# Optimization experiments

Measured on AMD Instinct MI355X. Metric: run time of the kernel, lower is better.

The kernel has to match this reference:

```python
import jax, jax.numpy as jnp
import numpy as np

EPS = 1e-6

def _phi(x):
    # elu(x) + 1 feature map
    return jax.nn.elu(x) + 1.0

def setup_inputs() -> dict:
    key = jax.random.key(0)
    kq, kk, kv = jax.random.split(key, 3)
    N, L, S, H, D, M = 8, 4096, 4096, 8, 64, 64
    queries = jax.random.normal(kq, (N, L, H, D), dtype=jnp.float32)
    keys = jax.random.normal(kk, (N, S, H, D), dtype=jnp.float32)
    values = jax.random.normal(kv, (N, S, H, M), dtype=jnp.float32)
    key_mask = jnp.ones((N, S), dtype=jnp.float32)  # key_lengths.float_matrix
    return {"queries": queries, "keys": keys, "values": values, "key_mask": key_mask}

def reference(queries, keys, values, key_mask):
    Q = _phi(queries)                                   # [N,L,H,D]
    K = _phi(keys) * key_mask[:, :, None, None]         # [N,S,H,D]
    KV = jnp.einsum('nshd,nshm->nhmd', K, values)       # [N,H,M,D]
    Z = 1.0 / (jnp.einsum('nlhd,nhd->nlh', Q, K.sum(axis=1)) + EPS)  # [N,L,H]
    V = jnp.einsum('nlhd,nhmd,nlh->nlhm', Q, KV, Z)     # [N,L,H,M]
    return V
```

## Files before the change

kernel.cpp:

```cpp
#include <hip/hip_runtime.h>


#define SLEN 4096
#define LLEN 4096
#define NHTOT 64
#define HD   512
#define NSPLIT 8
#define EPSF 1e-6f

typedef short s16x8 __attribute__((ext_vector_type(8)));
typedef float f32x4 __attribute__((ext_vector_type(4)));

__device__ __forceinline__ float phi(float x) {
    return x > 0.0f ? x + 1.0f : __expf(x);
}

__device__ __forceinline__ void fma4(float4& a, float s, const float4& b) {
    a.x = fmaf(s, b.x, a.x);
    a.y = fmaf(s, b.y, a.y);
    a.z = fmaf(s, b.z, a.z);
    a.w = fmaf(s, b.w, a.w);
}

__device__ __forceinline__ void bsplit(float x, short& hi, short& lo) {
    const unsigned bx = __float_as_uint(x);
    hi = (short)(bx >> 16);
    const float hf = __uint_as_float(bx & 0xFFFF0000u);
    lo = (short)(__float_as_uint(x - hf) >> 16);
}

__global__ __launch_bounds__(256, 2)
void la_phase1(const float* __restrict__ Kg, const float* __restrict__ Vg,
               const float* __restrict__ maskg,
               float* __restrict__ KVp, float* __restrict__ Ksump) {
    __shared__ float smem[4][4096];
    __shared__ float ksb[16 * 64];

    const int tid  = threadIdx.x;
    const int w    = tid >> 6;
    const int lane = tid & 63;
    const int nh   = blockIdx.y;
    const int n    = nh >> 3;
    const int h    = nh & 7;
    const int sp   = blockIdx.x;

    const int sr4 = lane >> 4;
    const int c4  = (lane & 15) * 4;
    const int d0  = (lane & 7) * 8;
    const int m0  = (lane >> 3) * 8;

    float* kw = smem[w];
    float* vw = smem[w] + 2048;

    const size_t base = (size_t)n * SLEN * HD + (size_t)h * 64;
    const float* mrow = maskg + (size_t)n * SLEN;
    const int wrow0 = sp * 512 + w * 128;

    float4 acc[8][2];
    #pragma unroll
    for (int i = 0; i < 8; ++i) {
        acc[i][0] = make_float4(0.f, 0.f, 0.f, 0.f);
        acc[i][1] = make_float4(0.f, 0.f, 0.f, 0.f);
    }
    float4 ksp = make_float4(0.f, 0.f, 0.f, 0.f);

    float4 pk[8], pv[8];
    float  pm[8];
    #pragma unroll
    for (int u = 0; u < 8; ++u) {
        const int s = wrow0 + sr4 + u * 4;
        const size_t g = base + (size_t)s * HD + c4;
        pk[u] = *(const float4*)(Kg + g);
        pv[u] = *(const float4*)(Vg + g);
        pm[u] = mrow[s];
    }

    #pragma unroll
    for (int t = 0; t < 4; ++t) {
        #pragma unroll
        for (int u = 0; u < 8; ++u) {
            const int row = sr4 + u * 4;
            float4 kf = pk[u];
            const float mm = pm[u];
            kf.x = phi(kf.x) * mm;
            kf.y = phi(kf.y) * mm;
            kf.z = phi(kf.z) * mm;
            kf.w = phi(kf.w) * mm;
            ksp.x += kf.x; ksp.y += kf.y; ksp.z += kf.z; ksp.w += kf.w;
            *(float4*)&kw[row * 64 + c4] = kf;
            *(float4*)&vw[row * 64 + c4] = pv[u];
        }
        if (t < 3) {
            #pragma unroll
            for (int u = 0; u < 8; ++u) {
                const int s = wrow0 + (t + 1) * 32 + sr4 + u * 4;
                const size_t g = base + (size_t)s * HD + c4;
                pk[u] = *(const float4*)(Kg + g);
                pv[u] = *(const float4*)(Vg + g);
                pm[u] = mrow[s];
            }
        }
        #pragma unroll 4
        for (int s = 0; s < 32; ++s) {
            const float4 ka = *(const float4*)&kw[s * 64 + d0];
            const float4 kz = *(const float4*)&kw[s * 64 + d0 + 4];
            const float4 va = *(const float4*)&vw[s * 64 + m0];
            const float4 vz = *(const float4*)&vw[s * 64 + m0 + 4];
            fma4(acc[0][0], ka.x, va); fma4(acc[0][1], ka.x, vz);
            fma4(acc[1][0], ka.y, va); fma4(acc[1][1], ka.y, vz);
            fma4(acc[2][0], ka.z, va); fma4(acc[2][1], ka.z, vz);
            fma4(acc[3][0], ka.w, va); fma4(acc[3][1], ka.w, vz);
            fma4(acc[4][0], kz.x, va); fma4(acc[4][1], kz.x, vz);
            fma4(acc[5][0], kz.y, va); fma4(acc[5][1], kz.y, vz);
            fma4(acc[6][0], kz.z, va); fma4(acc[6][1], kz.z, vz);
            fma4(acc[7][0], kz.w, va); fma4(acc[7][1], kz.w, vz);
        }
    }

    *(float4*)&ksb[(w * 4 + sr4) * 64 + c4] = ksp;

    #pragma unroll
    for (int di = 0; di < 8; ++di) {
        *(float4*)&smem[w][(d0 + di) * 64 + m0]     = acc[di][0];
        *(float4*)&smem[w][(d0 + di) * 64 + m0 + 4] = acc[di][1];
    }
    __syncthreads();

    float* outp = KVp + ((size_t)sp * NHTOT + nh) * 4096;
    #pragma unroll
    for (int j = 0; j < 4; ++j) {
        const int f = (j * 256 + tid) * 4;
        float4 a  = *(const float4*)&smem[0][f];
        const float4 b1 = *(const float4*)&smem[1][f];
        const float4 b2 = *(const float4*)&smem[2][f];
        const float4 b3 = *(const float4*)&smem[3][f];
        a.x += b1.x + b2.x + b3.x;
        a.y += b1.y + b2.y + b3.y;
        a.z += b1.z + b2.z + b3.z;
        a.w += b1.w + b2.w + b3.w;
        *(float4*)&outp[f] = a;
    }
    if (tid < 64) {
        float ssum = 0.f;
        #pragma unroll
        for (int r = 0; r < 16; ++r) ssum += ksb[r * 64 + tid];
        Ksump[((size_t)sp * NHTOT + nh) * 64 + tid] = ssum;
    }
}

__global__ __launch_bounds__(256)
void la_reduce(const float* __restrict__ KVp, const float* __restrict__ Ksump,
               short* __restrict__ KVThi, short* __restrict__ KVTlo,
               float* __restrict__ Ksum) {
    __shared__ float ld[64 * 20];

    const int nh  = blockIdx.y;
    const int mb  = blockIdx.x * 16;
    const int tid = threadIdx.x;

    const int d    = tid >> 2;
    const int moff = (tid & 3) * 4;
    float4 a = make_float4(0.f, 0.f, 0.f, 0.f);
    #pragma unroll
    for (int s = 0; s < NSPLIT; ++s) {
        const float4 v = *(const float4*)&KVp[((size_t)s * NHTOT + nh) * 4096 + d * 64 + mb + moff];
        a.x += v.x; a.y += v.y; a.z += v.z; a.w += v.w;
    }
    *(float4*)&ld[d * 20 + moff] = a;
    __syncthreads();

    const int mloc = tid >> 4;
    const int d0   = (tid & 15) * 4;
    short hi4[4], lo4[4];
    #pragma unroll
    for (int i = 0; i < 4; ++i)
        bsplit(ld[(d0 + i) * 20 + mloc], hi4[i], lo4[i]);
    const size_t o = (size_t)nh * 4096 + (mb + mloc) * 64 + d0;
    *(short4*)&KVThi[o] = *(short4*)hi4;
    *(short4*)&KVTlo[o] = *(short4*)lo4;

    if (blockIdx.x == 0 && tid < 64) {
        float b = 0.f;
        #pragma unroll
        for (int s = 0; s < NSPLIT; ++s)
            b += Ksump[((size_t)s * NHTOT + nh) * 64 + tid];
        Ksum[nh * 64 + tid] = b;
    }
}

__global__ __launch_bounds__(256)
void la_phase2(const float* __restrict__ Qg,
               const short* __restrict__ KVThi, const short* __restrict__ KVTlo,
               const float* __restrict__ Ksum, float* __restrict__ Og) {
    const int tid  = threadIdx.x;
    const int w    = tid >> 6;
    const int lane = tid & 63;
    const int nh   = blockIdx.y;
    const int n    = nh >> 3;
    const int h    = nh & 7;
    const int l0   = blockIdx.x * 128 + w * 32;

    const int r  = lane & 15;
    const int g4 = lane >> 4;

    const short* bhp = KVThi + (size_t)nh * 4096;
    const short* blp = KVTlo + (size_t)nh * 4096;
    const float* ksp = Ksum + nh * 64;

    f32x4 acc[2][4];
    #pragma unroll
    for (int t = 0; t < 2; ++t)
        #pragma unroll
        for (int u = 0; u < 4; ++u)
            acc[t][u] = (f32x4){0.f, 0.f, 0.f, 0.f};
    float den[2] = {0.f, 0.f};

    #pragma unroll
    for (int g = 0; g < 2; ++g) {
        const int db = g * 32 + g4 * 8;

        s16x8 Bh[4], Bl[4];
        #pragma unroll
        for (int u = 0; u < 4; ++u) {
            Bh[u] = *(const s16x8*)&bhp[(u * 16 + r) * 64 + db];
            Bl[u] = *(const s16x8*)&blp[(u * 16 + r) * 64 + db];
        }
        const float4 k0 = *(const float4*)&ksp[db];
        const float4 k1 = *(const float4*)&ksp[db + 4];

        #pragma unroll
        for (int t = 0; t < 2; ++t) {
            const float* qrow = Qg + ((size_t)(n * LLEN + l0 + t * 16 + r) * 8 + h) * 64 + db;
            float4 q0 = *(const float4*)qrow;
            float4 q1 = *(const float4*)(qrow + 4);
            q0.x = phi(q0.x); q0.y = phi(q0.y); q0.z = phi(q0.z); q0.w = phi(q0.w);
            q1.x = phi(q1.x); q1.y = phi(q1.y); q1.z = phi(q1.z); q1.w = phi(q1.w);

            float dn = den[t];
            dn = fmaf(q0.x, k0.x, dn); dn = fmaf(q0.y, k0.y, dn);
            dn = fmaf(q0.z, k0.z, dn); dn = fmaf(q0.w, k0.w, dn);
            dn = fmaf(q1.x, k1.x, dn); dn = fmaf(q1.y, k1.y, dn);
            dn = fmaf(q1.z, k1.z, dn); dn = fmaf(q1.w, k1.w, dn);
            den[t] = dn;

            s16x8 Ah, Al;
            {
                short hh, ll;
                bsplit(q0.x, hh, ll); Ah[0] = hh; Al[0] = ll;
                bsplit(q0.y, hh, ll); Ah[1] = hh; Al[1] = ll;
                bsplit(q0.z, hh, ll); Ah[2] = hh; Al[2] = ll;
                bsplit(q0.w, hh, ll); Ah[3] = hh; Al[3] = ll;
                bsplit(q1.x, hh, ll); Ah[4] = hh; Al[4] = ll;
                bsplit(q1.y, hh, ll); Ah[5] = hh; Al[5] = ll;
                bsplit(q1.z, hh, ll); Ah[6] = hh; Al[6] = ll;
                bsplit(q1.w, hh, ll); Ah[7] = hh; Al[7] = ll;
            }
            #pragma unroll
            for (int u = 0; u < 4; ++u) {
                acc[t][u] = __builtin_amdgcn_mfma_f32_16x16x32_bf16(Ah, Bh[u], acc[t][u], 0, 0, 0);
                acc[t][u] = __builtin_amdgcn_mfma_f32_16x16x32_bf16(Ah, Bl[u], acc[t][u], 0, 0, 0);
                acc[t][u] = __builtin_amdgcn_mfma_f32_16x16x32_bf16(Al, Bh[u], acc[t][u], 0, 0, 0);
            }
        }
    }

    #pragma unroll
    for (int t = 0; t < 2; ++t) {
        den[t] += __shfl_xor(den[t], 16, 64);
        den[t] += __shfl_xor(den[t], 32, 64);
    }

    #pragma unroll
    for (int t = 0; t < 2; ++t) {
        #pragma unroll
        for (int k = 0; k < 4; ++k) {
            const int ro = g4 * 4 + k;
            const float dk = __shfl(den[t], ro, 64);
            const float z  = 1.0f / (dk + EPSF);
            const int l = l0 + t * 16 + ro;
            float* op = &Og[((size_t)(n * LLEN + l) * 8 + h) * 64 + r];
            #pragma unroll
            for (int u = 0; u < 4; ++u)
                op[u * 16] = acc[t][u][k] * z;
        }
    }
}

extern "C" void kernel_launch(void* const* d_in, const int* in_sizes, int n_in,
                              void* d_out, int out_size, void* d_ws, size_t ws_size,
                              hipStream_t stream) {
    const float* Q    = (const float*)d_in[0];
    const float* K    = (const float*)d_in[1];
    const float* V    = (const float*)d_in[2];
    const float* mask = (const float*)d_in[3];
    float* out = (float*)d_out;

    float* KVp   = (float*)d_ws;
    float* Ksump = KVp + (size_t)NSPLIT * NHTOT * 4096;
    float* Ksum  = Ksump + (size_t)NSPLIT * NHTOT * 64;
    short* KVThi = (short*)(Ksum + NHTOT * 64);
    short* KVTlo = KVThi + (size_t)NHTOT * 4096;

    dim3 g1(NSPLIT, NHTOT);
    la_phase1<<<g1, 256, 0, stream>>>(K, V, mask, KVp, Ksump);

    dim3 gr(4, NHTOT);
    la_reduce<<<gr, 256, 0, stream>>>(KVp, Ksump, KVThi, KVTlo, Ksum);

    dim3 g2(LLEN / 128, NHTOT);
    la_phase2<<<g2, 256, 0, stream>>>(Q, KVThi, KVTlo, Ksum, out);
}
```

Measured before the change: 249.7 us.

## Compute phase-1 K^T V with split-bf16 MFMA instead of scalar FMA

The phase-1 kernel now converts phi(K) and V into hi/lo bf16 pairs and stores them transposed in a swizzled shared-memory layout. It then accumulates the KV outer product with three bf16 MFMA 16x16x32 instructions per tile (hi*hi, hi*lo, lo*hi) in place of the fp32 FMA loop. This moves the dominant reduction onto the matrix cores and approximates fp32 accuracy with a 3-term split, at the cost of extra packing work and shared-memory traffic. Accuracy drops slightly because the lo*lo term is left out.

New measurement: 239.3 us. 4.2% less time.

```diff
diff --git a/kernel.cpp b/kernel.cpp
--- a/kernel.cpp
+++ b/kernel.cpp
@@ -15,13 +15,12 @@
     return x > 0.0f ? x + 1.0f : __expf(x);
 }
 
-__device__ __forceinline__ void fma4(float4& a, float s, const float4& b) {
-    a.x = fmaf(s, b.x, a.x);
-    a.y = fmaf(s, b.y, a.y);
-    a.z = fmaf(s, b.z, a.z);
-    a.w = fmaf(s, b.w, a.w);
-}
-
+__device__ __forceinline__ unsigned pack_hi2(float a, float b) {
+    return (__float_as_uint(a) >> 16) | (__float_as_uint(b) & 0xFFFF0000u);
+}
+__device__ __forceinline__ float bres(float x) {
+    return x - __uint_as_float(__float_as_uint(x) & 0xFFFF0000u);
+}
 __device__ __forceinline__ void bsplit(float x, short& hi, short& lo) {
     const unsigned bx = __float_as_uint(x);
     hi = (short)(bx >> 16);
@@ -44,106 +43,138 @@
     const int h    = nh & 7;
     const int sp   = blockIdx.x;
 
-    const int sr4 = lane >> 4;
-    const int c4  = (lane & 15) * 4;
-    const int d0  = (lane & 7) * 8;
-    const int m0  = (lane >> 3) * 8;
-
-    float* kw = smem[w];
-    float* vw = smem[w] + 2048;
+    const int r  = lane & 15;
+    const int a  = lane >> 4;
+    const int c4 = r * 4;
+
+    char* const wbase = (char*)&smem[w][0];
+    char* const kthi = wbase;
+    char* const ktlo = wbase + 4096;
+    char* const vthi = wbase + 8192;
+    char* const vtlo = wbase + 12288;
 
     const size_t base = (size_t)n * SLEN * HD + (size_t)h * 64;
     const float* mrow = maskg + (size_t)n * SLEN;
     const int wrow0 = sp * 512 + w * 128;
 
-    float4 acc[8][2];
-    #pragma unroll
-    for (int i = 0; i < 8; ++i) {
-        acc[i][0] = make_float4(0.f, 0.f, 0.f, 0.f);
-        acc[i][1] = make_float4(0.f, 0.f, 0.f, 0.f);
-    }
+    const int woff0 = ((((a >> 1) ^ (r & 3)) << 4) | ((a & 1) << 3));
+    const int rkey  = (r >> 2) & 3;
+
+    f32x4 acc[4][4];
+    #pragma unroll
+    for (int i = 0; i < 4; ++i)
+        #pragma unroll
+        for (int j = 0; j < 4; ++j)
+            acc[i][j] = (f32x4){0.f, 0.f, 0.f, 0.f};
     float4 ksp = make_float4(0.f, 0.f, 0.f, 0.f);
 
-    float4 pk[8], pv[8];
-    float  pm[8];
-    #pragma unroll
-    for (int u = 0; u < 8; ++u) {
-        const int s = wrow0 + sr4 + u * 4;
-        const size_t g = base + (size_t)s * HD + c4;
-        pk[u] = *(const float4*)(Kg + g);
-        pv[u] = *(const float4*)(Vg + g);
-        pm[u] = mrow[s];
-    }
+    float4 pk[2][4], pv[2][4];
+    float  pm[2][4];
+    #pragma unroll
+    for (int u = 0; u < 2; ++u)
+        #pragma unroll
+        for (int j = 0; j < 4; ++j) {
+            const int s = wrow0 + u * 16 + a * 4 + j;
+            const size_t g = base + (size_t)s * HD + c4;
+            pk[u][j] = *(const float4*)(Kg + g);
+            pv[u][j] = *(const float4*)(Vg + g);
+            pm[u][j] = mrow[s];
+        }
 
     #pragma unroll
     for (int t = 0; t < 4; ++t) {
         #pragma unroll
-        for (int u = 0; u < 8; ++u) {
-            const int row = sr4 + u * 4;
-            float4 kf = pk[u];
-            const float mm = pm[u];
-            kf.x = phi(kf.x) * mm;
-            kf.y = phi(kf.y) * mm;
-            kf.z = phi(kf.z) * mm;
-            kf.w = phi(kf.w) * mm;
-            ksp.x += kf.x; ksp.y += kf.y; ksp.z += kf.z; ksp.w += kf.w;
-            *(float4*)&kw[row * 64 + c4] = kf;
-            *(float4*)&vw[row * 64 + c4] = pv[u];
+        for (int u = 0; u < 2; ++u) {
+            float4 kf[4];
+            #pragma unroll
+            for (int j = 0; j < 4; ++j) {
+                float4 kq = pk[u][j];
+                const float mm = pm[u][j];
+                kq.x = phi(kq.x) * mm; kq.y = phi(kq.y) * mm;
+                kq.z = phi(kq.z) * mm; kq.w = phi(kq.w) * mm;
+                kf[j] = kq;
+                ksp.x += kq.x; ksp.y += kq.y; ksp.z += kq.z; ksp.w += kq.w;
+            }
+            const int wo = woff0 ^ (u << 5);
+            #pragma unroll
+            for (int i = 0; i < 4; ++i) {
+                const int doff = r * 256 + i * 64 + wo;
+                const float k0 = (&kf[0].x)[i], k1 = (&kf[1].x)[i];
+                const float k2 = (&kf[2].x)[i], k3 = (&kf[3].x)[i];
+                *(uint2*)(kthi + doff) = make_uint2(pack_hi2(k0, k1), pack_hi2(k2, k3));
+                *(uint2*)(ktlo + doff) = make_uint2(pack_hi2(bres(k0), bres(k1)),
+                                                   pack_hi2(bres(k2), bres(k3)));
+                const float v0 = (&pv[u][0].x)[i], v1 = (&pv[u][1].x)[i];
+                const float v2 = (&pv[u][2].x)[i], v3 = (&pv[u][3].x)[i];
+                *(uint2*)(vthi + doff) = make_uint2(pack_hi2(v0, v1), pack_hi2(v2, v3));
+                *(uint2*)(vtlo + doff) = make_uint2(pack_hi2(bres(v0), bres(v1)),
+                                                   pack_hi2(bres(v2), bres(v3)));
+            }
         }
         if (t < 3) {
             #pragma unroll
-            for (int u = 0; u < 8; ++u) {
-                const int s = wrow0 + (t + 1) * 32 + sr4 + u * 4;
-                const size_t g = base + (size_t)s * HD + c4;
-                pk[u] = *(const float4*)(Kg + g);
-                pv[u] = *(const float4*)(Vg + g);
-                pm[u] = mrow[s];
-            }
-        }
-        #pragma unroll 4
-        for (int s = 0; s < 32; ++s) {
-            const float4 ka = *(const float4*)&kw[s * 64 + d0];
-            const float4 kz = *(const float4*)&kw[s * 64 + d0 + 4];
-            const float4 va = *(const float4*)&vw[s * 64 + m0];
-            const float4 vz = *(const float4*)&vw[s * 64 + m0 + 4];
-            fma4(acc[0][0], ka.x, va); fma4(acc[0][1], ka.x, vz);
-            fma4(acc[1][0], ka.y, va); fma4(acc[1][1], ka.y, vz);
-            fma4(acc[2][0], ka.z, va); fma4(acc[2][1], ka.z, vz);
-            fma4(acc[3][0], ka.w, va); fma4(acc[3][1], ka.w, vz);
-            fma4(acc[4][0], kz.x, va); fma4(acc[4][1], kz.x, vz);
-            fma4(acc[5][0], kz.y, va); fma4(acc[5][1], kz.y, vz);
-            fma4(acc[6][0], kz.z, va); fma4(acc[6][1], kz.z, vz);
-            fma4(acc[7][0], kz.w, va); fma4(acc[7][1], kz.w, vz);
-        }
-    }
-
-    *(float4*)&ksb[(w * 4 + sr4) * 64 + c4] = ksp;
-
-    #pragma unroll
-    for (int di = 0; di < 8; ++di) {
-        *(float4*)&smem[w][(d0 + di) * 64 + m0]     = acc[di][0];
-        *(float4*)&smem[w][(d0 + di) * 64 + m0 + 4] = acc[di][1];
-    }
+            for (int u = 0; u < 2; ++u)
+                #pragma unroll
+                for (int j = 0; j < 4; ++j) {
+                    const int s = wrow0 + (t + 1) * 32 + u * 16 + a * 4 + j;
+                    const size_t g = base + (size_t)s * HD + c4;
+                    pk[u][j] = *(const float4*)(Kg + g);
+                    pv[u][j] = *(const float4*)(Vg + g);
+                    pm[u][j] = mrow[s];
+                }
+        }
+        s16x8 Ah[4], Al[4];
+        const int cho = (a ^ rkey) << 4;
+        #pragma unroll
+        for (int dt = 0; dt < 4; ++dt) {
+            const int off = dt * 1024 + r * 64 + cho;
+            Ah[dt] = *(const s16x8*)(kthi + off);
+            Al[dt] = *(const s16x8*)(ktlo + off);
+        }
+        #pragma unroll
+        for (int mt = 0; mt < 4; ++mt) {
+            const int off = mt * 1024 + r * 64 + cho;
+            const s16x8 Bh = *(const s16x8*)(vthi + off);
+            const s16x8 Bl = *(const s16x8*)(vtlo + off);
+            #pragma unroll
+            for (int dt = 0; dt < 4; ++dt) {
+                acc[dt][mt] = __builtin_amdgcn_mfma_f32_16x16x32_bf16(Ah[dt], Bh, acc[dt][mt], 0, 0, 0);
+                acc[dt][mt] = __builtin_amdgcn_mfma_f32_16x16x32_bf16(Ah[dt], Bl, acc[dt][mt], 0, 0, 0);
+                acc[dt][mt] = __builtin_amdgcn_mfma_f32_16x16x32_bf16(Al[dt], Bh, acc[dt][mt], 0, 0, 0);
+            }
+        }
+    }
+
+    *(float4*)&ksb[(w * 4 + a) * 64 + c4] = ksp;
+
+    float* pw = &smem[w][0];
+    #pragma unroll
+    for (int dt = 0; dt < 4; ++dt)
+        #pragma unroll
+        for (int mt = 0; mt < 4; ++mt)
+            #pragma unroll
+            for (int p = 0; p < 4; ++p)
+                pw[(dt * 16 + a * 4 + p) * 64 + mt * 16 + r] = acc[dt][mt][p];
     __syncthreads();
 
     float* outp = KVp + ((size_t)sp * NHTOT + nh) * 4096;
     #pragma unroll
     for (int j = 0; j < 4; ++j) {
         const int f = (j * 256 + tid) * 4;
-        float4 a  = *(const float4*)&smem[0][f];
+        float4 s0  = *(const float4*)&smem[0][f];
         const float4 b1 = *(const float4*)&smem[1][f];
         const float4 b2 = *(const float4*)&smem[2][f];
         const float4 b3 = *(const float4*)&smem[3][f];
-        a.x += b1.x + b2.x + b3.x;
-        a.y += b1.y + b2.y + b3.y;
-        a.z += b1.z + b2.z + b3.z;
-        a.w += b1.w + b2.w + b3.w;
-        *(float4*)&outp[f] = a;
+        s0.x += b1.x + b2.x + b3.x;
+        s0.y += b1.y + b2.y + b3.y;
+        s0.z += b1.z + b2.z + b3.z;
+        s0.w += b1.w + b2.w + b3.w;
+        *(float4*)&outp[f] = s0;
     }
     if (tid < 64) {
         float ssum = 0.f;
         #pragma unroll
-        for (int r = 0; r < 16; ++r) ssum += ksb[r * 64 + tid];
+        for (int rr = 0; rr < 16; ++rr) ssum += ksb[rr * 64 + tid];
         Ksump[((size_t)sp * NHTOT + nh) * 64 + tid] = ssum;
     }
 }
```
